# Kernel tuning notes

Measured on AMD Instinct MI355X. Metric: run time of the kernel, lower is better.

## Reference

```python
import jax, jax.numpy as jnp
import numpy as np


def setup_inputs() -> dict:
    key = jax.random.key(0)
    k1, k2, k3 = jax.random.split(key, 3)
    B, L, H, E = 2, 2048, 16, 64
    queries = jax.random.normal(k1, (B, L, H, E), dtype=jnp.float32)
    keys = jax.random.normal(k2, (B, L, H, E), dtype=jnp.float32)
    values = jax.random.normal(k3, (B, L, H, E), dtype=jnp.float32)
    a1 = jnp.ones((), dtype=jnp.float32)
    a2 = jnp.ones((), dtype=jnp.float32)
    return {"queries": queries, "keys": keys, "values": values, "a1": a1, "a2": a2}


def reference(queries, keys, values, a1, a2):
    # ASSAAttention forward (eval mode: dropout is identity)
    B, L, H, E = queries.shape
    scale = 1.0 / jnp.sqrt(jnp.asarray(E, queries.dtype))
    # shared QK scores: [B, H, L, S]
    qk_scores = jnp.einsum('blhe,bshe->bhls', queries, keys) * scale
    # sparse path: squared-ReLU weighting
    ssa_scores = jax.nn.relu(qk_scores) ** 2
    ssa_output = jnp.einsum('bhls,bshd->blhd', ssa_scores, values)
    # dense path: softmax weighting
    dsa_scores = jax.nn.softmax(qk_scores, axis=-1)
    dsa_output = jnp.einsum('bhls,bshd->blhd', dsa_scores, values)
    # scalar blend with softmax over (a1, a2)
    w1 = jnp.exp(a1)
    w2 = jnp.exp(a2)
    alpha1 = w1 / (w1 + w2)
    alpha2 = w2 / (w1 + w2)
    return alpha1 * ssa_output + alpha2 * dsa_output
```

## Files before the change

kernel.cpp:

```cpp
#include <hip/hip_runtime.h>
#include <hip/hip_bf16.h>

typedef __attribute__((ext_vector_type(8))) short short8;
typedef __attribute__((ext_vector_type(4))) short short4v;
typedef __attribute__((ext_vector_type(4))) float f32x4;
typedef __attribute__((ext_vector_type(4))) unsigned uint4v;

#define LOG2E 1.4426950408889634f
#define ILN2SQ 0.4804530139182014f

__device__ __forceinline__ unsigned packbf2(float a, float b) {
  __hip_bfloat162 h = __float22bfloat162_rn(make_float2(a, b));
  return *reinterpret_cast<unsigned*>(&h);
}
__device__ __forceinline__ int swz(int row) {
  return ((row & 7) << 4) ^ (((row >> 3) & 3) << 5);
}
__device__ __forceinline__ void gload16(const void* g, void* l) {
  __builtin_amdgcn_global_load_lds(
      (const __attribute__((address_space(1))) unsigned int*)g,
      (__attribute__((address_space(3))) unsigned int*)l, 16, 0, 0);
}

__global__ __launch_bounds__(256) void assa_prep(
    const float* __restrict__ K, const float* __restrict__ V, char* __restrict__ WS)
{
  constexpr int L = 2048, RS = 1024, E = 64;
  char* KP = WS;
  char* VTP = WS + (size_t)8 * 1024 * 1024;
  __shared__ float tile[64][65];
  const int tid = threadIdx.x;

  if (blockIdx.x < 1024) {
    const int gid = blockIdx.x * 256 + tid;
    const int rid = gid >> 2;
    const int e0 = (gid & 3) * 16;
    const int bh = rid >> 11, s = rid & 2047;
    const int b = bh >> 4, h = bh & 15;
    const float* kr = K + ((size_t)b * L + s) * RS + h * E + e0;
    const float4 u0 = *(const float4*)(kr);
    const float4 u1 = *(const float4*)(kr + 4);
    const float4 u2 = *(const float4*)(kr + 8);
    const float4 u3 = *(const float4*)(kr + 12);
    uint4v w0, w1;
    w0[0] = packbf2(u0.x, u0.y); w0[1] = packbf2(u0.z, u0.w);
    w0[2] = packbf2(u1.x, u1.y); w0[3] = packbf2(u1.z, u1.w);
    w1[0] = packbf2(u2.x, u2.y); w1[1] = packbf2(u2.z, u2.w);
    w1[2] = packbf2(u3.x, u3.y); w1[3] = packbf2(u3.z, u3.w);
    char* dst = KP + (size_t)rid * 128;
    const int sz = swz(s);
    *(uint4v*)(dst + ((e0 * 2) ^ sz)) = w0;
    *(uint4v*)(dst + ((e0 * 2 + 16) ^ sz)) = w1;
  } else {
    const int bx = blockIdx.x - 1024;
    const int bh = bx >> 5, t5 = bx & 31;
    const int b = bh >> 4, h = bh & 15;
    const float* vb = V + ((size_t)b * L + t5 * 64) * RS + h * E;
    {
      const int key = tid >> 2, e0 = (tid & 3) * 16;
      const float* vr = vb + (size_t)key * RS + e0;
      const float4 u0 = *(const float4*)(vr);
      const float4 u1 = *(const float4*)(vr + 4);
      const float4 u2 = *(const float4*)(vr + 8);
      const float4 u3 = *(const float4*)(vr + 12);
      float* tr = &tile[key][e0];
      tr[0] = u0.x; tr[1] = u0.y; tr[2] = u0.z; tr[3] = u0.w;
      tr[4] = u1.x; tr[5] = u1.y; tr[6] = u1.z; tr[7] = u1.w;
      tr[8] = u2.x; tr[9] = u2.y; tr[10] = u2.z; tr[11] = u2.w;
      tr[12] = u3.x; tr[13] = u3.y; tr[14] = u3.z; tr[15] = u3.w;
    }
    __syncthreads();
    const int e = tid >> 2, p0 = (tid & 3) * 16;
    const int gg = p0 >> 4;
    uint4v w0, w1;
    #pragma unroll
    for (int i = 0; i < 4; ++i) {
      const int pa = 2 * i, pb = 2 * i + 1;
      const int k_a = ((pa >> 2) & 3) * 16 + gg * 4 + (pa & 3);
      const int k_b = ((pb >> 2) & 3) * 16 + gg * 4 + (pb & 3);
      w0[i] = packbf2(tile[k_a][e], tile[k_b][e]);
    }
    #pragma unroll
    for (int i = 0; i < 4; ++i) {
      const int pa = 8 + 2 * i, pb = 9 + 2 * i;
      const int k_a = ((pa >> 2) & 3) * 16 + gg * 4 + (pa & 3);
      const int k_b = ((pb >> 2) & 3) * 16 + gg * 4 + (pb & 3);
      w1[i] = packbf2(tile[k_a][e], tile[k_b][e]);
    }
    char* dst = VTP + ((size_t)bx * 64 + e) * 128;
    const int sz = swz(e);
    *(uint4v*)(dst + ((p0 * 2) ^ sz)) = w0;
    *(uint4v*)(dst + ((p0 * 2 + 16) ^ sz)) = w1;
  }
}

__global__ __launch_bounds__(256, 4) void assa_fused(
    const float* __restrict__ Q, const char* __restrict__ WS,
    const float* __restrict__ A1, const float* __restrict__ A2,
    float* __restrict__ O)
{
  constexpr int L = 2048, H = 16, E = 64, RS = H * E;

  __shared__ __align__(16) char Kb[2 * 8192];
  __shared__ __align__(16) char Vb[2 * 8192];

  const int t = threadIdx.x;
  const int wv = t >> 6;
  const int lane = t & 63;
  const int g = lane >> 4;
  const int c = lane & 15;

  const int bh = blockIdx.x;
  const int q0 = blockIdx.y * 64;
  const int b = bh >> 4;
  const int h = bh & 15;

  const float* qb = Q + (size_t)b * L * RS + (size_t)h * E;
  float* ob = O + (size_t)b * L * RS + (size_t)h * E;
  const char* KP = WS;
  const char* VTP = WS + (size_t)8 * 1024 * 1024;

  const float a1 = A1[0], a2 = A2[0];
  const float am = fmaxf(a1, a2);
  const float e1 = expf(a1 - am), e2 = expf(a2 - am);
  const float alpha1 = (e1 / (e1 + e2)) * ILN2SQ;
  const float alpha2 = e2 / (e1 + e2);

  short8 aq[2];
  {
    const float qs = 0.125f * LOG2E;
    const float* qr = qb + (size_t)(q0 + wv * 16 + c) * RS;
    #pragma unroll
    for (int ks = 0; ks < 2; ++ks) {
      const float4 u0 = *(const float4*)(qr + ks * 32 + g * 8);
      const float4 u1 = *(const float4*)(qr + ks * 32 + g * 8 + 4);
      unsigned p0 = packbf2(u0.x * qs, u0.y * qs);
      unsigned p1 = packbf2(u0.z * qs, u0.w * qs);
      unsigned p2 = packbf2(u1.x * qs, u1.y * qs);
      unsigned p3 = packbf2(u1.z * qs, u1.w * qs);
      short8 f;
      f[0] = (short)(p0 & 0xffff); f[1] = (short)(p0 >> 16);
      f[2] = (short)(p1 & 0xffff); f[3] = (short)(p1 >> 16);
      f[4] = (short)(p2 & 0xffff); f[5] = (short)(p2 >> 16);
      f[6] = (short)(p3 & 0xffff); f[7] = (short)(p3 >> 16);
      aq[ks] = f;
    }
  }

  int ka[8];
  #pragma unroll
  for (int kt = 0; kt < 4; ++kt) {
    const int row = kt * 16 + c;
    const int s = swz(row);
    ka[kt * 2 + 0] = (row * 128 + g * 16) ^ s;
    ka[kt * 2 + 1] = (row * 128 + 64 + g * 16) ^ s;
  }
  int va[8];
  #pragma unroll
  for (int et = 0; et < 4; ++et) {
    const int row = et * 16 + c;
    const int s = swz(row);
    va[et * 2 + 0] = (row * 128 + g * 32) ^ s;
    va[et * 2 + 1] = (row * 128 + g * 32 + 16) ^ s;
  }

  const f32x4 zero4 = {0.0f, 0.0f, 0.0f, 0.0f};
  f32x4 od[4], os[4];
  #pragma unroll
  for (int i = 0; i < 4; ++i) { od[i] = zero4; os[i] = zero4; }
  float psum = 0.0f;

  const char* kp = KP + (size_t)bh * (2048 * 128) + wv * 1024 + lane * 16;
  const char* vp = VTP + (size_t)bh * (2048 * 128) + wv * 1024 + lane * 16;
  char* kd = Kb + wv * 1024;
  char* vd = Vb + wv * 1024;

#define STAGE(TOFF, HALF)                              \
  do {                                                 \
    gload16(kp + (TOFF), kd + (HALF));                 \
    gload16(kp + (TOFF) + 4096, kd + (HALF) + 4096);   \
    gload16(vp + (TOFF), vd + (HALF));                 \
    gload16(vp + (TOFF) + 4096, vd + (HALF) + 4096);   \
  } while (0)

#define COMPUTE(OFS)                                                                 \
  do {                                                                               \
    f32x4 acc[4];                                                                    \
    _Pragma("unroll")                                                                \
    for (int i = 0; i < 4; ++i) acc[i] = zero4;                                      \
    _Pragma("unroll")                                                                \
    for (int kt = 0; kt < 4; ++kt) {                                                 \
      const short8 kf0 = *(const short8*)(Kb + ka[kt * 2 + 0] + (OFS));              \
      const short8 kf1 = *(const short8*)(Kb + ka[kt * 2 + 1] + (OFS));              \
      acc[kt] = __builtin_amdgcn_mfma_f32_16x16x32_bf16(kf0, aq[0], acc[kt], 0, 0, 0);\
      acc[kt] = __builtin_amdgcn_mfma_f32_16x16x32_bf16(kf1, aq[1], acc[kt], 0, 0, 0);\
    }                                                                                \
    short8 vv[4], vw[4];                                                             \
    _Pragma("unroll")                                                                \
    for (int et = 0; et < 4; ++et) {                                                 \
      vv[et] = *(const short8*)(Vb + va[et * 2 + 0] + (OFS));                        \
      vw[et] = *(const short8*)(Vb + va[et * 2 + 1] + (OFS));                        \
    }                                                                                \
    _Pragma("unroll")                                                                \
    for (int kt = 0; kt < 4; ++kt) {                                                 \
      const float x0 = __builtin_amdgcn_exp2f(acc[kt][0]);                           \
      const float x1 = __builtin_amdgcn_exp2f(acc[kt][1]);                           \
      const float x2 = __builtin_amdgcn_exp2f(acc[kt][2]);                           \
      const float x3 = __builtin_amdgcn_exp2f(acc[kt][3]);                           \
      psum += (x0 + x1) + (x2 + x3);                                                 \
      const float r0 = fmaxf(acc[kt][0], 0.0f), r1 = fmaxf(acc[kt][1], 0.0f);        \
      const float r2 = fmaxf(acc[kt][2], 0.0f), r3 = fmaxf(acc[kt][3], 0.0f);        \
      union { unsigned u[2]; short4v v; } pdu, psu;                                  \
      pdu.u[0] = packbf2(x0, x1); pdu.u[1] = packbf2(x2, x3);                        \
      psu.u[0] = packbf2(r0 * r0, r1 * r1); psu.u[1] = packbf2(r2 * r2, r3 * r3);    \
      const short4v pd = pdu.v, ps = psu.v;                                          \
      _Pragma("unroll")                                                              \
      for (int et = 0; et < 4; ++et) {                                               \
        const short8 vsrc = (kt < 2) ? vv[et] : vw[et];                              \
        short4v vf;                                                                  \
        if (kt & 1) { vf[0] = vsrc[4]; vf[1] = vsrc[5]; vf[2] = vsrc[6]; vf[3] = vsrc[7]; } \
        else        { vf[0] = vsrc[0]; vf[1] = vsrc[1]; vf[2] = vsrc[2]; vf[3] = vsrc[3]; } \
        od[et] = __builtin_amdgcn_mfma_f32_16x16x16bf16_1k(vf, pd, od[et], 0, 0, 0); \
        os[et] = __builtin_amdgcn_mfma_f32_16x16x16bf16_1k(vf, ps, os[et], 0, 0, 0); \
      }                                                                              \
    }                                                                                \
  } while (0)

  STAGE(0, 0);
  __syncthreads();
  size_t toff = 8192;
  for (int it = 0; it < 32; it += 2) {
    STAGE(toff, 8192); toff += 8192;
    COMPUTE(0);
    __syncthreads();
    if (it + 2 < 32) { STAGE(toff, 0); toff += 8192; }
    COMPUTE(8192);
    __syncthreads();
  }
#undef STAGE
#undef COMPUTE

  float l = psum;
  l += __shfl_xor(l, 16);
  l += __shfl_xor(l, 32);

  const float wd = alpha2 / l;
  float* orow = ob + (size_t)(q0 + wv * 16 + c) * RS;
  #pragma unroll
  for (int et = 0; et < 4; ++et) {
    float4 o;
    o.x = alpha1 * os[et][0] + wd * od[et][0];
    o.y = alpha1 * os[et][1] + wd * od[et][1];
    o.z = alpha1 * os[et][2] + wd * od[et][2];
    o.w = alpha1 * os[et][3] + wd * od[et][3];
    *(float4*)(orow + et * 16 + g * 4) = o;
  }
}

extern "C" void kernel_launch(void* const* d_in, const int* in_sizes, int n_in,
                              void* d_out, int out_size, void* d_ws, size_t ws_size,
                              hipStream_t stream) {
  const float* q = (const float*)d_in[0];
  const float* k = (const float*)d_in[1];
  const float* v = (const float*)d_in[2];
  const float* a1 = (const float*)d_in[3];
  const float* a2 = (const float*)d_in[4];
  float* out = (float*)d_out;
  char* ws = (char*)d_ws;

  assa_prep<<<2048, 256, 0, stream>>>(k, v, ws);
  dim3 grid(32, 32);
  assa_fused<<<grid, 256, 0, stream>>>(q, ws, a1, a2, out);
}
```

Measured before the change: 93.79 us.

## Process two 16-row query sets per wave to reuse K/V tiles

Each wave now handles 32 query rows (two 16-row sets) instead of 16, so every block covers 128 queries and the grid's query dimension is halved. Each K/V fragment read from LDS feeds MFMAs for both sets, which halves the global and LDS traffic for K/V per query. Register use roughly doubles for accumulators, and launch bounds drop to 2 blocks per CU, which lowers occupancy and halves the block count to 512.

Measured after the change: 89.34 us. 4.7% less time.

```diff
diff --git a/kernel.cpp b/kernel.cpp
--- a/kernel.cpp
+++ b/kernel.cpp
@@ -94,7 +94,7 @@
   }
 }
 
-__global__ __launch_bounds__(256, 4) void assa_fused(
+__global__ __launch_bounds__(256, 2) void assa_fused(
     const float* __restrict__ Q, const char* __restrict__ WS,
     const float* __restrict__ A1, const float* __restrict__ A2,
     float* __restrict__ O)
@@ -111,7 +111,7 @@
   const int c = lane & 15;
 
   const int bh = blockIdx.x;
-  const int q0 = blockIdx.y * 64;
+  const int q0 = blockIdx.y * 128;
   const int b = bh >> 4;
   const int h = bh & 15;
 
@@ -126,24 +126,27 @@
   const float alpha1 = (e1 / (e1 + e2)) * ILN2SQ;
   const float alpha2 = e2 / (e1 + e2);
 
-  short8 aq[2];
+  short8 aqA[2], aqB[2];
   {
     const float qs = 0.125f * LOG2E;
-    const float* qr = qb + (size_t)(q0 + wv * 16 + c) * RS;
     #pragma unroll
-    for (int ks = 0; ks < 2; ++ks) {
-      const float4 u0 = *(const float4*)(qr + ks * 32 + g * 8);
-      const float4 u1 = *(const float4*)(qr + ks * 32 + g * 8 + 4);
-      unsigned p0 = packbf2(u0.x * qs, u0.y * qs);
-      unsigned p1 = packbf2(u0.z * qs, u0.w * qs);
-      unsigned p2 = packbf2(u1.x * qs, u1.y * qs);
-      unsigned p3 = packbf2(u1.z * qs, u1.w * qs);
-      short8 f;
-      f[0] = (short)(p0 & 0xffff); f[1] = (short)(p0 >> 16);
-      f[2] = (short)(p1 & 0xffff); f[3] = (short)(p1 >> 16);
-      f[4] = (short)(p2 & 0xffff); f[5] = (short)(p2 >> 16);
-      f[6] = (short)(p3 & 0xffff); f[7] = (short)(p3 >> 16);
-      aq[ks] = f;
+    for (int setb = 0; setb < 2; ++setb) {
+      const float* qr = qb + (size_t)(q0 + wv * 32 + setb * 16 + c) * RS;
+      #pragma unroll
+      for (int ks = 0; ks < 2; ++ks) {
+        const float4 u0 = *(const float4*)(qr + ks * 32 + g * 8);
+        const float4 u1 = *(const float4*)(qr + ks * 32 + g * 8 + 4);
+        unsigned p0 = packbf2(u0.x * qs, u0.y * qs);
+        unsigned p1 = packbf2(u0.z * qs, u0.w * qs);
+        unsigned p2 = packbf2(u1.x * qs, u1.y * qs);
+        unsigned p3 = packbf2(u1.z * qs, u1.w * qs);
+        short8 f;
+        f[0] = (short)(p0 & 0xffff); f[1] = (short)(p0 >> 16);
+        f[2] = (short)(p1 & 0xffff); f[3] = (short)(p1 >> 16);
+        f[4] = (short)(p2 & 0xffff); f[5] = (short)(p2 >> 16);
+        f[6] = (short)(p3 & 0xffff); f[7] = (short)(p3 >> 16);
+        if (setb) aqB[ks] = f; else aqA[ks] = f;
+      }
     }
   }
 
@@ -165,10 +168,10 @@
   }
 
   const f32x4 zero4 = {0.0f, 0.0f, 0.0f, 0.0f};
-  f32x4 od[4], os[4];
-  #pragma unroll
-  for (int i = 0; i < 4; ++i) { od[i] = zero4; os[i] = zero4; }
-  float psum = 0.0f;
+  f32x4 odA[4], osA[4], odB[4], osB[4];
+  #pragma unroll
+  for (int i = 0; i < 4; ++i) { odA[i] = zero4; osA[i] = zero4; odB[i] = zero4; osB[i] = zero4; }
+  float psumA = 0.0f, psumB = 0.0f;
 
   const char* kp = KP + (size_t)bh * (2048 * 128) + wv * 1024 + lane * 16;
   const char* vp = VTP + (size_t)bh * (2048 * 128) + wv * 1024 + lane * 16;
@@ -183,33 +186,17 @@
     gload16(vp + (TOFF) + 4096, vd + (HALF) + 4096);   \
   } while (0)
 
-#define COMPUTE(OFS)                                                                 \
+#define PROC(ACC, OD, OS, PSUM)                                                      \
   do {                                                                               \
-    f32x4 acc[4];                                                                    \
-    _Pragma("unroll")                                                                \
-    for (int i = 0; i < 4; ++i) acc[i] = zero4;                                      \
     _Pragma("unroll")                                                                \
     for (int kt = 0; kt < 4; ++kt) {                                                 \
-      const short8 kf0 = *(const short8*)(Kb + ka[kt * 2 + 0] + (OFS));              \
-      const short8 kf1 = *(const short8*)(Kb + ka[kt * 2 + 1] + (OFS));              \
-      acc[kt] = __builtin_amdgcn_mfma_f32_16x16x32_bf16(kf0, aq[0], acc[kt], 0, 0, 0);\
-      acc[kt] = __builtin_amdgcn_mfma_f32_16x16x32_bf16(kf1, aq[1], acc[kt], 0, 0, 0);\
-    }                                                                                \
-    short8 vv[4], vw[4];                                                             \
-    _Pragma("unroll")                                                                \
-    for (int et = 0; et < 4; ++et) {                                                 \
-      vv[et] = *(const short8*)(Vb + va[et * 2 + 0] + (OFS));                        \
-      vw[et] = *(const short8*)(Vb + va[et * 2 + 1] + (OFS));                        \
-    }                                                                                \
-    _Pragma("unroll")                                                                \
-    for (int kt = 0; kt < 4; ++kt) {                                                 \
-      const float x0 = __builtin_amdgcn_exp2f(acc[kt][0]);                           \
-      const float x1 = __builtin_amdgcn_exp2f(acc[kt][1]);                           \
-      const float x2 = __builtin_amdgcn_exp2f(acc[kt][2]);                           \
-      const float x3 = __builtin_amdgcn_exp2f(acc[kt][3]);                           \
-      psum += (x0 + x1) + (x2 + x3);                                                 \
-      const float r0 = fmaxf(acc[kt][0], 0.0f), r1 = fmaxf(acc[kt][1], 0.0f);        \
-      const float r2 = fmaxf(acc[kt][2], 0.0f), r3 = fmaxf(acc[kt][3], 0.0f);        \
+      const float x0 = __builtin_amdgcn_exp2f(ACC[kt][0]);                           \
+      const float x1 = __builtin_amdgcn_exp2f(ACC[kt][1]);                           \
+      const float x2 = __builtin_amdgcn_exp2f(ACC[kt][2]);                           \
+      const float x3 = __builtin_amdgcn_exp2f(ACC[kt][3]);                           \
+      PSUM += (x0 + x1) + (x2 + x3);                                                 \
+      const float r0 = fmaxf(ACC[kt][0], 0.0f), r1 = fmaxf(ACC[kt][1], 0.0f);        \
+      const float r2 = fmaxf(ACC[kt][2], 0.0f), r3 = fmaxf(ACC[kt][3], 0.0f);        \
       union { unsigned u[2]; short4v v; } pdu, psu;                                  \
       pdu.u[0] = packbf2(x0, x1); pdu.u[1] = packbf2(x2, x3);                        \
       psu.u[0] = packbf2(r0 * r0, r1 * r1); psu.u[1] = packbf2(r2 * r2, r3 * r3);    \
@@ -220,10 +207,34 @@
         short4v vf;                                                                  \
         if (kt & 1) { vf[0] = vsrc[4]; vf[1] = vsrc[5]; vf[2] = vsrc[6]; vf[3] = vsrc[7]; } \
         else        { vf[0] = vsrc[0]; vf[1] = vsrc[1]; vf[2] = vsrc[2]; vf[3] = vsrc[3]; } \
-        od[et] = __builtin_amdgcn_mfma_f32_16x16x16bf16_1k(vf, pd, od[et], 0, 0, 0); \
-        os[et] = __builtin_amdgcn_mfma_f32_16x16x16bf16_1k(vf, ps, os[et], 0, 0, 0); \
+        OD[et] = __builtin_amdgcn_mfma_f32_16x16x16bf16_1k(vf, pd, OD[et], 0, 0, 0); \
+        OS[et] = __builtin_amdgcn_mfma_f32_16x16x16bf16_1k(vf, ps, OS[et], 0, 0, 0); \
       }                                                                              \
     }                                                                                \
+  } while (0)
+
+#define COMPUTE(OFS)                                                                 \
+  do {                                                                               \
+    f32x4 aA[4], aB[4];                                                              \
+    _Pragma("unroll")                                                                \
+    for (int i = 0; i < 4; ++i) { aA[i] = zero4; aB[i] = zero4; }                    \
+    _Pragma("unroll")                                                                \
+    for (int kt = 0; kt < 4; ++kt) {                                                 \
+      const short8 kf0 = *(const short8*)(Kb + ka[kt * 2 + 0] + (OFS));              \
+      const short8 kf1 = *(const short8*)(Kb + ka[kt * 2 + 1] + (OFS));              \
+      aA[kt] = __builtin_amdgcn_mfma_f32_16x16x32_bf16(kf0, aqA[0], aA[kt], 0, 0, 0);\
+      aA[kt] = __builtin_amdgcn_mfma_f32_16x16x32_bf16(kf1, aqA[1], aA[kt], 0, 0, 0);\
+      aB[kt] = __builtin_amdgcn_mfma_f32_16x16x32_bf16(kf0, aqB[0], aB[kt], 0, 0, 0);\
+      aB[kt] = __builtin_amdgcn_mfma_f32_16x16x32_bf16(kf1, aqB[1], aB[kt], 0, 0, 0);\
+    }                                                                                \
+    short8 vv[4], vw[4];                                                             \
+    _Pragma("unroll")                                                                \
+    for (int et = 0; et < 4; ++et) {                                                 \
+      vv[et] = *(const short8*)(Vb + va[et * 2 + 0] + (OFS));                        \
+      vw[et] = *(const short8*)(Vb + va[et * 2 + 1] + (OFS));                        \
+    }                                                                                \
+    PROC(aA, odA, osA, psumA);                                                       \
+    PROC(aB, odB, osB, psumB);                                                       \
   } while (0)
 
   STAGE(0, 0);
@@ -238,22 +249,33 @@
     __syncthreads();
   }
 #undef STAGE
+#undef PROC
 #undef COMPUTE
 
-  float l = psum;
-  l += __shfl_xor(l, 16);
-  l += __shfl_xor(l, 32);
-
-  const float wd = alpha2 / l;
-  float* orow = ob + (size_t)(q0 + wv * 16 + c) * RS;
+  float lA = psumA;
+  lA += __shfl_xor(lA, 16);
+  lA += __shfl_xor(lA, 32);
+  float lB = psumB;
+  lB += __shfl_xor(lB, 16);
+  lB += __shfl_xor(lB, 32);
+
+  const float wdA = alpha2 / lA;
+  const float wdB = alpha2 / lB;
+  float* orowA = ob + (size_t)(q0 + wv * 32 + c) * RS;
+  float* orowB = orowA + (size_t)16 * RS;
   #pragma unroll
   for (int et = 0; et < 4; ++et) {
-    float4 o;
-    o.x = alpha1 * os[et][0] + wd * od[et][0];
-    o.y = alpha1 * os[et][1] + wd * od[et][1];
-    o.z = alpha1 * os[et][2] + wd * od[et][2];
-    o.w = alpha1 * os[et][3] + wd * od[et][3];
-    *(float4*)(orow + et * 16 + g * 4) = o;
+    float4 oa, obv;
+    oa.x = alpha1 * osA[et][0] + wdA * odA[et][0];
+    oa.y = alpha1 * osA[et][1] + wdA * odA[et][1];
+    oa.z = alpha1 * osA[et][2] + wdA * odA[et][2];
+    oa.w = alpha1 * osA[et][3] + wdA * odA[et][3];
+    obv.x = alpha1 * osB[et][0] + wdB * odB[et][0];
+    obv.y = alpha1 * osB[et][1] + wdB * odB[et][1];
+    obv.z = alpha1 * osB[et][2] + wdB * odB[et][2];
+    obv.w = alpha1 * osB[et][3] + wdB * odB[et][3];
+    *(float4*)(orowA + et * 16 + g * 4) = oa;
+    *(float4*)(orowB + et * 16 + g * 4) = obv;
   }
 }
 
@@ -269,6 +291,6 @@
   char* ws = (char*)d_ws;
 
   assa_prep<<<2048, 256, 0, stream>>>(k, v, ws);
-  dim3 grid(32, 32);
+  dim3 grid(32, 16);
   assa_fused<<<grid, 256, 0, stream>>>(q, ws, a1, a2, out);
 }
```
